# Kernel tuning notes

Measured on AMD Instinct MI355X. Metric: run time of the kernel, lower is better.

Reference implementation:

```python
import jax, jax.numpy as jnp
import numpy as np

N_NODES = 20000   # nodes
IN_DEG = 8        # fixed in-degree -> E = N*D edges, T = E*D triplets
MSG = 64          # message_size


def _build_indices():
    rng = np.random.default_rng(0)
    E = N_NODES * IN_DEG
    # edge e: row[e] -> col[e]; node j's incoming edges are j*D : (j+1)*D
    row = rng.integers(0, N_NODES, size=E).astype(np.int32)          # source j of edge (j->i)
    # triplets of edge e=(j->i): all edges k->j, i.e. incoming edges of row[e]
    idx_kj = (row[:, None] * IN_DEG + np.arange(IN_DEG, dtype=np.int32)[None, :]).reshape(-1)
    idx_ji = np.repeat(np.arange(E, dtype=np.int32), IN_DEG)
    idx_j = np.repeat(row, IN_DEG)   # pooled-to node for each triplet
    return idx_kj, idx_ji, idx_j, E


def setup_inputs() -> dict:
    idx_kj, idx_ji, idx_j, E = _build_indices()
    key = jax.random.key(0)
    ks = jax.random.split(key, 8)
    s1 = 1.0 / np.sqrt(2 * MSG)
    s2 = 1.0 / np.sqrt(MSG)
    return {
        "messages": jax.random.normal(ks[0], (E, MSG), jnp.float32),
        "r": jax.random.normal(ks[1], (E, 2), jnp.float32),
        "W1": jax.random.uniform(ks[2], (2 * MSG, MSG), jnp.float32, -s1, s1),
        "b1": jax.random.uniform(ks[3], (MSG,), jnp.float32, -s1, s1),
        "W2": jax.random.uniform(ks[4], (MSG, MSG), jnp.float32, -s2, s2),
        "b2": jax.random.uniform(ks[5], (MSG,), jnp.float32, -s2, s2),
        "W3": jax.random.uniform(ks[6], (MSG, 1), jnp.float32, -s2, s2),
        "b3": jax.random.uniform(ks[7], (1,), jnp.float32, -s2, s2),
        "idx_kj": jnp.asarray(idx_kj),
        "idx_ji": jnp.asarray(idx_ji),
        "idx_j": jnp.asarray(idx_j),
        "num_nodes": N_NODES,
    }


def reference(messages, r, W1, b1, W2, b2, W3, b3, idx_kj, idx_ji, idx_j, num_nodes):
    # gather triplet messages and run the 3-layer MLP (Linear/Softplus/Linear/Softplus/Linear)
    h = jnp.concatenate([messages[idx_kj], messages[idx_ji]], axis=1)  # [T, 2M]
    h = jax.nn.softplus(h @ W1 + b1)
    h = jax.nn.softplus(h @ W2 + b2)
    m_ijk = h @ W3 + b3                                                # [T, 1]
    # dyad[t,k,j] = r[idx_ji][t,k] * r[idx_kj][t,j]  (einsum 'ij,ik->ikj')
    rk = r[idx_kj]                                                     # [T, 2]
    rj = r[idx_ji]                                                     # [T, 2]
    dyad = (rj[:, :, None] * rk[:, None, :]).reshape(-1, 4)            # [T, 4]
    temp = m_ijk * dyad                                                # [T, 4]
    # global_mean_pool over idx_j
    s = jax.ops.segment_sum(temp, idx_j, num_segments=num_nodes)       # [N, 4]
    cnt = jax.ops.segment_sum(jnp.ones((temp.shape[0],), temp.dtype), idx_j,
                              num_segments=num_nodes)
    out = s / jnp.maximum(cnt, 1.0)[:, None]
    return out.reshape(-1, 2, 2)
```

## Files before the change

kernel.cpp:

```cpp
#include <hip/hip_runtime.h>

typedef _Float16 half8 __attribute__((ext_vector_type(8)));
typedef __fp16 fp16x2 __attribute__((ext_vector_type(2)));
typedef float floatx4 __attribute__((ext_vector_type(4)));

#define MSGW 64
#define DEG 8

__device__ __forceinline__ float softplus_f(float x) {
    float ax = __builtin_fabsf(x);
    float t  = __builtin_amdgcn_exp2f(-1.44269504089f * ax);
    float l  = 0.69314718056f * __builtin_amdgcn_logf(1.0f + t);
    return fmaxf(x, 0.0f) + l;
}

__device__ __forceinline__ half8 cvt8(const float* p) {
    float4 x = *(const float4*)p;
    float4 y = *(const float4*)(p + 4);
    fp16x2 p0 = __builtin_amdgcn_cvt_pkrtz(x.x, x.y);
    fp16x2 p1 = __builtin_amdgcn_cvt_pkrtz(x.z, x.w);
    fp16x2 p2 = __builtin_amdgcn_cvt_pkrtz(y.x, y.y);
    fp16x2 p3 = __builtin_amdgcn_cvt_pkrtz(y.z, y.w);
    half8 h;
    h[0] = (_Float16)p0[0]; h[1] = (_Float16)p0[1];
    h[2] = (_Float16)p1[0]; h[3] = (_Float16)p1[1];
    h[4] = (_Float16)p2[0]; h[5] = (_Float16)p2[1];
    h[6] = (_Float16)p3[0]; h[7] = (_Float16)p3[1];
    return h;
}

__device__ __forceinline__ half8 sp8(half8 z) {
    half8 h;
#pragma unroll
    for (int j = 0; j < 8; j += 2) {
        fp16x2 pk = __builtin_amdgcn_cvt_pkrtz(softplus_f((float)z[j]),
                                               softplus_f((float)z[j + 1]));
        h[j] = (_Float16)pk[0]; h[j + 1] = (_Float16)pk[1];
    }
    return h;
}

template<int CTRL>
__device__ __forceinline__ float dpp_addf(float x) {
    int y = __builtin_amdgcn_update_dpp(0, __float_as_int(x), CTRL, 0xF, 0xF, true);
    return x + __int_as_float(y);
}
__device__ __forceinline__ float red16(float x) {
    x = dpp_addf<0xB1>(x);
    x = dpp_addf<0x4E>(x);
    x = dpp_addf<0x141>(x);
    x = dpp_addf<0x140>(x);
    return x;
}
__device__ __forceinline__ float red8(float x) {
    x = dpp_addf<0xB1>(x);
    x = dpp_addf<0x4E>(x);
    x = dpp_addf<0x141>(x);
    return x;
}

__global__ void prep_kernel(const float* __restrict__ W1, const float* __restrict__ W2,
                            _Float16* __restrict__ W1f, _Float16* __restrict__ W2f,
                            float4* __restrict__ zs, int nz4) {
    const int g = blockIdx.x * 256 + threadIdx.x;
    const int stride = gridDim.x * 256;
    float4 z = {0.f, 0.f, 0.f, 0.f};
    for (int i = g; i < nz4; i += stride) zs[i] = z;
    for (int idx = g; idx < 16 * 512; idx += stride) {
        int f = idx >> 9, lane = (idx >> 3) & 63, j = idx & 7;
        int nt = f >> 1, ks = f & 1;
        int k = ks * 32 + (lane >> 4) * 8 + j;
        int np = nt * 16 + (lane & 15);
        float v = (np < 64) ? W1[k * 64 + np] : W1[(64 + k) * 64 + (np - 64)];
        W1f[idx] = (_Float16)v;
    }
    for (int idx = g; idx < 8 * 512; idx += stride) {
        int f = idx >> 9, lane = (idx >> 3) & 63, j = idx & 7;
        int nt = f >> 1, ks = f & 1;
        int k = ks * 32 + (lane >> 4) * 8 + j;
        int n = nt * 16 + (lane & 15);
        W2f[idx] = (_Float16)W2[k * 64 + n];
    }
}

__global__ __launch_bounds__(256, 2)
void edge_proj_kernel(const float* __restrict__ messages,
                      const _Float16* __restrict__ W1f, const float* __restrict__ b1,
                      _Float16* __restrict__ PQ, int E)
{
    __shared__ __align__(16) _Float16 lw1x[16 * 512];
    __shared__ __align__(16) _Float16 lrep[4][16 * 132];

    const int tid = threadIdx.x;
    for (int i = tid; i < 1024; i += 256)
        *(half8*)&lw1x[i * 8] = *(const half8*)&W1f[i * 8];
    __syncthreads();

    const int wave = tid >> 6;
    const int lane = tid & 63;
    const int s = lane & 15;
    const int q = lane >> 4;
    const int e0 = (blockIdx.x * 4 + wave) * 16;
    if (e0 >= E) return;

    float b1v[4];
#pragma unroll
    for (int nt = 0; nt < 4; ++nt) b1v[nt] = b1[nt * 16 + s];

    int er = e0 + s; if (er >= E) er = E - 1;
    const float* mp = messages + (size_t)er * MSGW + q * 8;
    half8 af0 = cvt8(mp);
    half8 af1 = cvt8(mp + 32);

    floatx4 acc[8];
#pragma unroll
    for (int nt = 0; nt < 4; ++nt) { floatx4 z = {0.f, 0.f, 0.f, 0.f}; acc[nt] = z; }
#pragma unroll
    for (int nt = 4; nt < 8; ++nt) {
        float bv = b1v[nt - 4];
        floatx4 iv = {bv, bv, bv, bv};
        acc[nt] = iv;
    }
#pragma unroll
    for (int nt = 0; nt < 8; ++nt) {
        half8 bf0 = *(const half8*)&lw1x[(nt * 2 + 0) * 512 + lane * 8];
        acc[nt] = __builtin_amdgcn_mfma_f32_16x16x32_f16(af0, bf0, acc[nt], 0, 0, 0);
        half8 bf1 = *(const half8*)&lw1x[(nt * 2 + 1) * 512 + lane * 8];
        acc[nt] = __builtin_amdgcn_mfma_f32_16x16x32_f16(af1, bf1, acc[nt], 0, 0, 0);
    }

    _Float16* rep = lrep[wave];
#pragma unroll
    for (int nt = 0; nt < 8; ++nt)
#pragma unroll
        for (int rr = 0; rr < 4; ++rr)
            rep[(q * 4 + rr) * 132 + nt * 16 + s] = (_Float16)acc[nt][rr];
    __asm__ volatile("s_waitcnt lgkmcnt(0)" ::: "memory");

#pragma unroll
    for (int cc = 0; cc < 4; ++cc) {
        int c = cc * 64 + lane;
        int rrow = c >> 4, c16 = c & 15;
        half8 v = *(const half8*)&rep[rrow * 132 + c16 * 8];
        int eg = e0 + rrow;
        if (eg < E)
            *(half8*)&PQ[(size_t)eg * 128 + c16 * 8] = v;
    }
}

__global__ __launch_bounds__(256, 3)
void triplet_mlp2_kernel(const _Float16* __restrict__ PQ,
                         const float* __restrict__ r2,
                         const _Float16* __restrict__ W2f,
                         const float* __restrict__ b2,
                         const float* __restrict__ W3, const float* __restrict__ b3,
                         const int* __restrict__ idx_kj,
                         float* __restrict__ sacc, float* __restrict__ cnt,
                         int nChunks)
{
    const int tid = threadIdx.x;
    const int wave = tid >> 6;
    const int lane = tid & 63;
    const int s = lane & 15;
    const int q = lane >> 4;

    half8 w2f[2][4];
#pragma unroll
    for (int nt = 0; nt < 4; ++nt) {
        w2f[0][nt] = *(const half8*)&W2f[(nt * 2 + 0) * 512 + lane * 8];
        w2f[1][nt] = *(const half8*)&W2f[(nt * 2 + 1) * 512 + lane * 8];
    }
    float b2v[4], w3v[4];
#pragma unroll
    for (int nt = 0; nt < 4; ++nt) {
        b2v[nt] = b2[nt * 16 + s];
        w3v[nt] = W3[nt * 16 + s];
    }
    const float b3v = b3[0];
    const int aa = q >> 1;
    const int bperm_addr = (((s >> 2) << 4) + s) << 2;

    const int T = nChunks * 64;
    const int stride = gridDim.x * 64;

    int t = blockIdx.x * 64 + wave * 16 + s;
    int kj = idx_kj[t];
    int t1 = t + stride; int t1c = (t1 < T) ? t1 : 0;
    int kjn = idx_kj[t1c];

    const _Float16* pk0 = PQ + (size_t)kj * 128 + q * 8;
    const _Float16* pj0 = PQ + (size_t)(t >> 3) * 128 + 64 + q * 8;
    half8 p0 = *(const half8*)pk0;
    half8 p1 = *(const half8*)(pk0 + 32);
    half8 q0 = *(const half8*)pj0;
    half8 q1 = *(const half8*)(pj0 + 32);
    float2 rkv = *(const float2*)(r2 + (size_t)kj * 2);
    float rjv = r2[(size_t)(t >> 3) * 2 + aa];

    for (int chunk = blockIdx.x; chunk < nChunks; chunk += gridDim.x) {
        int t2 = t + 2 * stride; int t2c = (t2 < T) ? t2 : 0;
        const int kj2 = idx_kj[t2c];
        const _Float16* pkn = PQ + (size_t)kjn * 128 + q * 8;
        const _Float16* pjn = PQ + (size_t)(t1c >> 3) * 128 + 64 + q * 8;
        half8 np0 = *(const half8*)pkn;
        half8 np1 = *(const half8*)(pkn + 32);
        half8 nq0 = *(const half8*)pjn;
        half8 nq1 = *(const half8*)(pjn + 32);
        float2 nrk = *(const float2*)(r2 + (size_t)kjn * 2);
        float nrj = r2[(size_t)(t1c >> 3) * 2 + aa];

        const int ji = t >> 3;
        const int jn = kj >> 3;
        (void)ji;

        half8 z0 = p0 + q0;
        half8 z1 = p1 + q1;
        half8 a20 = sp8(z0);
        half8 a21 = sp8(z1);

        floatx4 acc2[4];
#pragma unroll
        for (int nt = 0; nt < 4; ++nt) {
            float bv = b2v[nt];
            floatx4 iv = {bv, bv, bv, bv};
            acc2[nt] = iv;
        }
#pragma unroll
        for (int nt = 0; nt < 4; ++nt) {
            acc2[nt] = __builtin_amdgcn_mfma_f32_16x16x32_f16(a20, w2f[0][nt], acc2[nt], 0, 0, 0);
            acc2[nt] = __builtin_amdgcn_mfma_f32_16x16x32_f16(a21, w2f[1][nt], acc2[nt], 0, 0, 0);
        }

        float part[4];
#pragma unroll
        for (int rr = 0; rr < 4; ++rr) {
            float p = 0.0f;
#pragma unroll
            for (int nt = 0; nt < 4; ++nt)
                p += softplus_f(acc2[nt][rr]) * w3v[nt];
            part[rr] = red16(p);
        }

        const int rsel = s & 3;
        float mm = part[0];
        mm = (rsel == 1) ? part[1] : mm;
        mm = (rsel == 2) ? part[2] : mm;
        mm = (rsel == 3) ? part[3] : mm;
        mm = __int_as_float(__builtin_amdgcn_ds_bpermute(bperm_addr, __float_as_int(mm)));
        mm += b3v;

        float c = mm * ((q & 1) ? rkv.y : rkv.x);
        c = red8(c);

        if ((s & 7) == 0) {
            const int bb = q & 1;
            atomicAdd(&sacc[(size_t)jn * 4 + aa * 2 + bb], rjv * c);
            if (q == 0) atomicAdd(&cnt[jn], 8.0f);
        }

        t += stride;
        kj = kjn; kjn = kj2;
        t1c = t2c;
        p0 = np0; p1 = np1; q0 = nq0; q1 = nq1;
        rkv = nrk; rjv = nrj;
    }
}

__global__ __launch_bounds__(256, 3)
void triplet_mlp_fb_kernel(const float* __restrict__ messages,
                           const float* __restrict__ r2,
                           const float* __restrict__ W1, const float* __restrict__ b1,
                           const float* __restrict__ W2, const float* __restrict__ b2,
                           const float* __restrict__ W3, const float* __restrict__ b3,
                           const int* __restrict__ idx_kj,
                           float* __restrict__ sacc, float* __restrict__ cnt,
                           int nChunks)
{
    __shared__ _Float16 lw1x[16 * 512];
    __shared__ _Float16 lw2x[8 * 512];
    __shared__ float lb1[64], lb2[64], lw3[64];
    __shared__ _Float16 lh[4][16 * 72];

    const int tid = threadIdx.x;
    for (int i = tid; i < 128 * 64; i += 256) {
        int k = i >> 6, n = i & 63;
        int ks = k >> 5, q = (k >> 3) & 3, j = k & 7;
        int nt = n >> 4, s = n & 15;
        lw1x[(nt * 4 + ks) * 512 + (q * 16 + s) * 8 + j] = (_Float16)W1[i];
    }
    for (int i = tid; i < 64 * 64; i += 256) {
        int k = i >> 6, n = i & 63;
        int ks = k >> 5, q = (k >> 3) & 3, j = k & 7;
        int nt = n >> 4, s = n & 15;
        lw2x[(nt * 2 + ks) * 512 + (q * 16 + s) * 8 + j] = (_Float16)W2[i];
    }
    if (tid < 64) { lb1[tid] = b1[tid]; lb2[tid] = b2[tid]; lw3[tid] = W3[tid]; }
    __syncthreads();

    const int wave = tid >> 6;
    const int lane = tid & 63;
    const int s = lane & 15;
    const int q = lane >> 4;
    const float b3v = b3[0];
    const int T = nChunks * 64;
    const int stride = gridDim.x * 64;

    _Float16* myh = lh[wave];

    int t = blockIdx.x * 64 + wave * 16 + s;
    int kj = (t < T) ? idx_kj[t] : 0;

    for (int chunk = blockIdx.x; chunk < nChunks; chunk += gridDim.x) {
        const int t_next = t + stride;
        const int kj_next = idx_kj[(t_next < T) ? t_next : 0];

        const int ji = t >> 3;
        const int jn = kj >> 3;

        const float* mk = messages + (size_t)kj * MSGW + q * 8;
        const float* mj = messages + (size_t)ji * MSGW + q * 8;
        half8 afr[4];
        afr[0] = cvt8(mk);
        afr[1] = cvt8(mk + 32);
        afr[2] = cvt8(mj);
        afr[3] = cvt8(mj + 32);

        const float rk0 = r2[(size_t)kj * 2];
        const float rk1 = r2[(size_t)kj * 2 + 1];

        floatx4 acc[4];
#pragma unroll
        for (int nt = 0; nt < 4; ++nt) {
            float bv = lb1[nt * 16 + s];
            floatx4 iv = {bv, bv, bv, bv};
            acc[nt] = iv;
        }
#pragma unroll
        for (int ks = 0; ks < 4; ++ks)
#pragma unroll
            for (int nt = 0; nt < 4; ++nt) {
                half8 bf = *(const half8*)&lw1x[(nt * 4 + ks) * 512 + lane * 8];
                acc[nt] = __builtin_amdgcn_mfma_f32_16x16x32_f16(afr[ks], bf, acc[nt], 0, 0, 0);
            }

#pragma unroll
        for (int nt = 0; nt < 4; ++nt)
#pragma unroll
            for (int rr = 0; rr < 4; ++rr)
                myh[(q * 4 + rr) * 72 + nt * 16 + s] = (_Float16)softplus_f(acc[nt][rr]);
        __asm__ volatile("s_waitcnt lgkmcnt(0)" ::: "memory");

        half8 a2[2];
        a2[0] = *(const half8*)&myh[s * 72 + q * 8];
        a2[1] = *(const half8*)&myh[s * 72 + 32 + q * 8];
        __asm__ volatile("" ::: "memory");

        floatx4 acc2[4];
#pragma unroll
        for (int nt = 0; nt < 4; ++nt) {
            float bv = lb2[nt * 16 + s];
            floatx4 iv = {bv, bv, bv, bv};
            acc2[nt] = iv;
        }
#pragma unroll
        for (int ks = 0; ks < 2; ++ks)
#pragma unroll
            for (int nt = 0; nt < 4; ++nt) {
                half8 bf = *(const half8*)&lw2x[(nt * 2 + ks) * 512 + lane * 8];
                acc2[nt] = __builtin_amdgcn_mfma_f32_16x16x32_f16(a2[ks], bf, acc2[nt], 0, 0, 0);
            }

        float part[4];
#pragma unroll
        for (int rr = 0; rr < 4; ++rr) {
            float p = 0.0f;
#pragma unroll
            for (int nt = 0; nt < 4; ++nt)
                p += softplus_f(acc2[nt][rr]) * lw3[nt * 16 + s];
            part[rr] = p;
        }
#pragma unroll
        for (int mask = 1; mask < 16; mask <<= 1)
#pragma unroll
            for (int rr = 0; rr < 4; ++rr)
                part[rr] += __shfl_xor(part[rr], mask, 16);

        const int srcl = (s >> 2) << 4;
        float mr[4];
#pragma unroll
        for (int rr = 0; rr < 4; ++rr)
            mr[rr] = __shfl(part[rr], srcl, 64);
        const int rsel = s & 3;
        float m_mine = mr[0];
        m_mine = (rsel == 1) ? mr[1] : m_mine;
        m_mine = (rsel == 2) ? mr[2] : m_mine;
        m_mine = (rsel == 3) ? mr[3] : m_mine;
        m_mine += b3v;

        float c = m_mine * ((q & 1) ? rk1 : rk0);
        c += __shfl_xor(c, 1, 16);
        c += __shfl_xor(c, 2, 16);
        c += __shfl_xor(c, 4, 16);

        if ((s & 7) == 0) {
            const int aa = q >> 1, bb = q & 1;
            const float rj = r2[(size_t)ji * 2 + aa];
            atomicAdd(&sacc[(size_t)jn * 4 + aa * 2 + bb], rj * c);
            if (q == 0) atomicAdd(&cnt[jn], 8.0f);
        }

        t = t_next;
        kj = kj_next;
    }
}

__global__ void finalize_kernel(const float* __restrict__ sacc, const float* __restrict__ cnt,
                                float* __restrict__ out, int n4) {
    int i = blockIdx.x * 256 + threadIdx.x;
    if (i < n4) {
        float c = cnt[i >> 2];
        out[i] = sacc[i] / fmaxf(c, 1.0f);
    }
}

extern "C" void kernel_launch(void* const* d_in, const int* in_sizes, int n_in,
                              void* d_out, int out_size, void* d_ws, size_t ws_size,
                              hipStream_t stream) {
    const float* messages = (const float*)d_in[0];
    const float* r2       = (const float*)d_in[1];
    const float* W1       = (const float*)d_in[2];
    const float* b1       = (const float*)d_in[3];
    const float* W2       = (const float*)d_in[4];
    const float* b2       = (const float*)d_in[5];
    const float* W3       = (const float*)d_in[6];
    const float* b3       = (const float*)d_in[7];
    const int* idx_kj     = (const int*)d_in[8];

    const int T = in_sizes[8];
    const int E = T / DEG;
    const int N = out_size / 4;
    float* sacc = (float*)d_ws;
    float* cntp = sacc + (size_t)N * 4;

    const int nChunks = T / 64;
    int grid = nChunks < 4096 ? nChunks : 4096;

    const size_t pqOff  = (((size_t)N * 5 * sizeof(float)) + 255) & ~(size_t)255;
    const size_t w1fOff = pqOff + (size_t)E * 128 * sizeof(_Float16);
    const size_t w2fOff = w1fOff + (size_t)16 * 512 * sizeof(_Float16);
    const size_t needWs = w2fOff + (size_t)8 * 512 * sizeof(_Float16);

    if (ws_size >= needWs) {
        _Float16* PQ  = (_Float16*)((char*)d_ws + pqOff);
        _Float16* W1f = (_Float16*)((char*)d_ws + w1fOff);
        _Float16* W2f = (_Float16*)((char*)d_ws + w2fOff);

        prep_kernel<<<48, 256, 0, stream>>>(W1, W2, W1f, W2f,
                                            (float4*)d_ws, (N * 5) / 4);

        const int tiles = (E + 15) / 16;
        const int epgrid = (tiles + 3) / 4;
        edge_proj_kernel<<<epgrid, 256, 0, stream>>>(messages, W1f, b1, PQ, E);

        triplet_mlp2_kernel<<<grid, 256, 0, stream>>>(PQ, r2, W2f, b2, W3, b3,
                                                      idx_kj, sacc, cntp, nChunks);
    } else {
        (void)hipMemsetAsync(d_ws, 0, (size_t)N * 5 * sizeof(float), stream);
        triplet_mlp_fb_kernel<<<grid, 256, 0, stream>>>(messages, r2, W1, b1, W2, b2, W3, b3,
                                                        idx_kj, sacc, cntp, nChunks);
    }

    const int n4 = N * 4;
    finalize_kernel<<<(n4 + 255) / 256, 256, 0, stream>>>(sacc, cntp, (float*)d_out, n4);
}
```

Measured before the change: 173.8 us.

## Fold weight prep into main kernels and fuse finalize via last-block counter

Removes the separate prep kernel: edge_proj now zeroes the accumulators and converts/swizzles W1 into LDS directly from fp32, and the triplet kernel builds its W2 fragments from fp32 W2 per thread. The finalize kernel is folded into the triplet kernel, where the last NFIN blocks wait on a global done counter and then compute the mean. Launch bounds go from 3 to 6 waves per SIMD, and softplus uses an fma. This cuts two kernel launches in exchange for spin-waiting blocks, extra per-block weight conversion work, and register pressure from the higher occupancy target.

```diff
diff --git a/kernel.cpp b/kernel.cpp
--- a/kernel.cpp
+++ b/kernel.cpp
@@ -10,8 +10,8 @@
 __device__ __forceinline__ float softplus_f(float x) {
     float ax = __builtin_fabsf(x);
     float t  = __builtin_amdgcn_exp2f(-1.44269504089f * ax);
-    float l  = 0.69314718056f * __builtin_amdgcn_logf(1.0f + t);
-    return fmaxf(x, 0.0f) + l;
+    float l  = __builtin_amdgcn_logf(1.0f + t);
+    return fmaf(0.69314718056f, l, fmaxf(x, 0.0f));
 }
 
 __device__ __forceinline__ half8 cvt8(const float* p) {
@@ -59,41 +59,30 @@
     return x;
 }
 
-__global__ void prep_kernel(const float* __restrict__ W1, const float* __restrict__ W2,
-                            _Float16* __restrict__ W1f, _Float16* __restrict__ W2f,
-                            float4* __restrict__ zs, int nz4) {
-    const int g = blockIdx.x * 256 + threadIdx.x;
-    const int stride = gridDim.x * 256;
-    float4 z = {0.f, 0.f, 0.f, 0.f};
-    for (int i = g; i < nz4; i += stride) zs[i] = z;
-    for (int idx = g; idx < 16 * 512; idx += stride) {
-        int f = idx >> 9, lane = (idx >> 3) & 63, j = idx & 7;
-        int nt = f >> 1, ks = f & 1;
-        int k = ks * 32 + (lane >> 4) * 8 + j;
-        int np = nt * 16 + (lane & 15);
-        float v = (np < 64) ? W1[k * 64 + np] : W1[(64 + k) * 64 + (np - 64)];
-        W1f[idx] = (_Float16)v;
-    }
-    for (int idx = g; idx < 8 * 512; idx += stride) {
-        int f = idx >> 9, lane = (idx >> 3) & 63, j = idx & 7;
-        int nt = f >> 1, ks = f & 1;
-        int k = ks * 32 + (lane >> 4) * 8 + j;
-        int n = nt * 16 + (lane & 15);
-        W2f[idx] = (_Float16)W2[k * 64 + n];
-    }
-}
-
 __global__ __launch_bounds__(256, 2)
 void edge_proj_kernel(const float* __restrict__ messages,
-                      const _Float16* __restrict__ W1f, const float* __restrict__ b1,
-                      _Float16* __restrict__ PQ, int E)
+                      const float* __restrict__ W1, const float* __restrict__ b1,
+                      _Float16* __restrict__ PQ, int E,
+                      float4* __restrict__ zs, int nz4)
 {
     __shared__ __align__(16) _Float16 lw1x[16 * 512];
     __shared__ __align__(16) _Float16 lrep[4][16 * 132];
 
     const int tid = threadIdx.x;
-    for (int i = tid; i < 1024; i += 256)
-        *(half8*)&lw1x[i * 8] = *(const half8*)&W1f[i * 8];
+
+    {
+        float4 z = {0.f, 0.f, 0.f, 0.f};
+        for (int i = blockIdx.x * 256 + tid; i < nz4; i += gridDim.x * 256) zs[i] = z;
+    }
+
+    for (int i = tid; i < 128 * 64; i += 256) {
+        int r = i >> 6, c = i & 63;
+        int k  = (r < 64) ? r : (r - 64);
+        int np = (r < 64) ? c : (64 + c);
+        int f  = (np >> 4) * 2 + (k >> 5);
+        int ln = ((k >> 3) & 3) * 16 + (np & 15);
+        lw1x[f * 512 + ln * 8 + (k & 7)] = (_Float16)W1[i];
+    }
     __syncthreads();
 
     const int wave = tid >> 6;
@@ -148,16 +137,20 @@
     }
 }
 
-__global__ __launch_bounds__(256, 3)
+#define NFIN 64
+
+__global__ __launch_bounds__(256, 6)
 void triplet_mlp2_kernel(const _Float16* __restrict__ PQ,
                          const float* __restrict__ r2,
-                         const _Float16* __restrict__ W2f,
+                         const float* __restrict__ W2,
                          const float* __restrict__ b2,
                          const float* __restrict__ W3, const float* __restrict__ b3,
                          const int* __restrict__ idx_kj,
                          float* __restrict__ sacc, float* __restrict__ cnt,
-                         int nChunks)
+                         int* __restrict__ done, float* __restrict__ out,
+                         int n4, int nChunks)
 {
+    __shared__ int lslice;
     const int tid = threadIdx.x;
     const int wave = tid >> 6;
     const int lane = tid & 63;
@@ -166,10 +159,15 @@
 
     half8 w2f[2][4];
 #pragma unroll
-    for (int nt = 0; nt < 4; ++nt) {
-        w2f[0][nt] = *(const half8*)&W2f[(nt * 2 + 0) * 512 + lane * 8];
-        w2f[1][nt] = *(const half8*)&W2f[(nt * 2 + 1) * 512 + lane * 8];
-    }
+    for (int ks = 0; ks < 2; ++ks)
+#pragma unroll
+        for (int nt = 0; nt < 4; ++nt) {
+            half8 h;
+#pragma unroll
+            for (int j = 0; j < 8; ++j)
+                h[j] = (_Float16)W2[(ks * 32 + q * 8 + j) * 64 + nt * 16 + s];
+            w2f[ks][nt] = h;
+        }
     float b2v[4], w3v[4];
 #pragma unroll
     for (int nt = 0; nt < 4; ++nt) {
@@ -209,9 +207,7 @@
         float2 nrk = *(const float2*)(r2 + (size_t)kjn * 2);
         float nrj = r2[(size_t)(t1c >> 3) * 2 + aa];
 
-        const int ji = t >> 3;
         const int jn = kj >> 3;
-        (void)ji;
 
         half8 z0 = p0 + q0;
         half8 z1 = p1 + q1;
@@ -263,6 +259,28 @@
         t1c = t2c;
         p0 = np0; p1 = np1; q0 = nq0; q1 = nq1;
         rkv = nrk; rjv = nrj;
+    }
+
+    __syncthreads();
+    if (tid == 0) {
+        __threadfence();
+        int prev = __hip_atomic_fetch_add(done, 1, __ATOMIC_ACQ_REL, __HIP_MEMORY_SCOPE_AGENT);
+        int sl = prev - ((int)gridDim.x - NFIN);
+        if (sl >= 0) {
+            while (__hip_atomic_load(done, __ATOMIC_ACQUIRE, __HIP_MEMORY_SCOPE_AGENT)
+                   < (int)gridDim.x)
+                __builtin_amdgcn_s_sleep(8);
+        }
+        lslice = sl;
+    }
+    __syncthreads();
+    const int sl = lslice;
+    if (sl >= 0) {
+        for (int i = sl * 256 + tid; i < n4; i += NFIN * 256) {
+            float sv = __hip_atomic_load(&sacc[i],      __ATOMIC_RELAXED, __HIP_MEMORY_SCOPE_AGENT);
+            float cv = __hip_atomic_load(&cnt[i >> 2],  __ATOMIC_RELAXED, __HIP_MEMORY_SCOPE_AGENT);
+            out[i] = sv / fmaxf(cv, 1.0f);
+        }
     }
 }
 
@@ -441,35 +459,32 @@
     const int N = out_size / 4;
     float* sacc = (float*)d_ws;
     float* cntp = sacc + (size_t)N * 4;
+    int*   done = (int*)(cntp + N);
 
     const int nChunks = T / 64;
     int grid = nChunks < 4096 ? nChunks : 4096;
-
-    const size_t pqOff  = (((size_t)N * 5 * sizeof(float)) + 255) & ~(size_t)255;
-    const size_t w1fOff = pqOff + (size_t)E * 128 * sizeof(_Float16);
-    const size_t w2fOff = w1fOff + (size_t)16 * 512 * sizeof(_Float16);
-    const size_t needWs = w2fOff + (size_t)8 * 512 * sizeof(_Float16);
-
-    if (ws_size >= needWs) {
-        _Float16* PQ  = (_Float16*)((char*)d_ws + pqOff);
-        _Float16* W1f = (_Float16*)((char*)d_ws + w1fOff);
-        _Float16* W2f = (_Float16*)((char*)d_ws + w2fOff);
-
-        prep_kernel<<<48, 256, 0, stream>>>(W1, W2, W1f, W2f,
-                                            (float4*)d_ws, (N * 5) / 4);
+    const int n4 = N * 4;
+
+    const int nz4 = (N * 5 + 4) / 4;
+    const size_t zBytes = (size_t)nz4 * 16;
+    const size_t pqOff  = (zBytes + 255) & ~(size_t)255;
+    const size_t needWs = pqOff + (size_t)E * 128 * sizeof(_Float16);
+
+    if (ws_size >= needWs && grid > NFIN) {
+        _Float16* PQ = (_Float16*)((char*)d_ws + pqOff);
 
         const int tiles = (E + 15) / 16;
         const int epgrid = (tiles + 3) / 4;
-        edge_proj_kernel<<<epgrid, 256, 0, stream>>>(messages, W1f, b1, PQ, E);
-
-        triplet_mlp2_kernel<<<grid, 256, 0, stream>>>(PQ, r2, W2f, b2, W3, b3,
-                                                      idx_kj, sacc, cntp, nChunks);
+        edge_proj_kernel<<<epgrid, 256, 0, stream>>>(messages, W1, b1, PQ, E,
+                                                     (float4*)d_ws, nz4);
+
+        triplet_mlp2_kernel<<<grid, 256, 0, stream>>>(PQ, r2, W2, b2, W3, b3,
+                                                      idx_kj, sacc, cntp, done,
+                                                      (float*)d_out, n4, nChunks);
     } else {
         (void)hipMemsetAsync(d_ws, 0, (size_t)N * 5 * sizeof(float), stream);
         triplet_mlp_fb_kernel<<<grid, 256, 0, stream>>>(messages, r2, W1, b1, W2, b2, W3, b3,
                                                         idx_kj, sacc, cntp, nChunks);
-    }
-
-    const int n4 = N * 4;
-    finalize_kernel<<<(n4 + 255) / 256, 256, 0, stream>>>(sacc, cntp, (float*)d_out, n4);
-}
+        finalize_kernel<<<(n4 + 255) / 256, 256, 0, stream>>>(sacc, cntp, (float*)d_out, n4);
+    }
+}
```

After: 523.0 us. 3.01x slower.
